# Performance work log

Measured on AMD Instinct MI355X. Metric: run time of the kernel, lower is better.

## Reference

```python
import jax, jax.numpy as jnp
import numpy as np

N, E, D, H, C, G = 20000, 160000, 128, 4, 3, 512
IN_F, EF = 74, 11


def setup_inputs():
    key = jax.random.key(0)
    ks = jax.random.split(key, 20)
    rn = lambda k, shape, s=0.05: jax.random.normal(k, shape, jnp.float32) * s
    return {
        "h0": rn(ks[0], (N, IN_F), 1.0),
        "e_f": rn(ks[1], (E, EF), 1.0),
        "src": jax.random.randint(ks[2], (E,), 0, N, jnp.int32),
        "dst": jax.random.randint(ks[3], (E,), 0, N, jnp.int32),
        "node_gid": jnp.sort(jax.random.randint(ks[4], (N,), 0, G, jnp.int32)),
        "num_graphs": G,
        "lin0_W": rn(ks[5], (H, IN_F, D)),
        "lin_W": rn(ks[6], (C - 1, H, D, D)),
        "We_W": rn(ks[7], (C, H, EF, D)),
        "Wq_W": rn(ks[8], (C, H, D, D)),
        "Wk_W": rn(ks[9], (C, H, D, D)),
        "Wv_W": rn(ks[10], (C, H, D, D)),
        "ln_g": jnp.ones((C, H, D), jnp.float32),
        "ln_b": jnp.zeros((C, H, D), jnp.float32),
        "out_W": rn(ks[11], (C, H * D, D)),
        "out_b": jnp.zeros((C, D), jnp.float32),
        "proj_W": rn(ks[12], (IN_F, D)),
        "proj_b": jnp.zeros((D,), jnp.float32),
        "gru_Wih0": rn(ks[13], (2, D, 3 * D)),
        "gru_Whh0": rn(ks[14], (2, D, 3 * D)),
        "gru_bih0": jnp.zeros((2, 3 * D), jnp.float32),
        "gru_bhh0": jnp.zeros((2, 3 * D), jnp.float32),
        "gru_Wih1": rn(ks[15], (2, 2 * D, 3 * D)),
        "gru_Whh1": rn(ks[16], (2, D, 3 * D)),
        "gru_bih1": jnp.zeros((2, 3 * D), jnp.float32),
        "gru_bhh1": jnp.zeros((2, 3 * D), jnp.float32),
    }


def _seg_mean(x, ids, n):
    s = jax.ops.segment_sum(x, ids, num_segments=n)
    c = jax.ops.segment_sum(jnp.ones((x.shape[0], 1), x.dtype), ids, num_segments=n)
    return s / jnp.maximum(c, 1.0)


def _layernorm(x, g, b, eps=1e-5):
    m = jnp.mean(x, -1, keepdims=True)
    v = jnp.var(x, -1, keepdims=True)
    return (x - m) * jax.lax.rsqrt(v + eps) * g + b


def _gat_head(h, ef_raw, src, dst, n, Wl, We, Wq, Wk, Wv, g, b):
    z = h @ Wl                                  # [N, D]
    ef = ef_raw @ We                            # [E, D]
    x = jnp.stack([z[src], z[dst], ef], axis=1)  # [E, 3, D]
    Q = jnp.einsum('eid,df->eif', x, Wq)
    K = jnp.einsum('eid,df->eif', x, Wk)
    V = jnp.einsum('eid,df->eif', x, Wv)
    attn = jax.nn.softmax(jnp.einsum('eid,ejd->eij', Q, K), axis=-1)  # [E,3,3]
    m = jnp.einsum('eij,ejd->ed', attn, V)      # (attn @ V).sum(1)
    h_new = _seg_mean(m, dst, n)                # mean over incoming edges
    return _layernorm(jax.nn.relu(h_new), g, b)


def _gru_dir(xs, Wih, Whh, bih, bhh, reverse):
    # xs: [T, B, in]; torch gate order r, z, n
    def step(h, x):
        gi = x @ Wih + bih
        gh = h @ Whh + bhh
        ir, iz, inn = jnp.split(gi, 3, axis=-1)
        hr, hz, hn = jnp.split(gh, 3, axis=-1)
        r = jax.nn.sigmoid(ir + hr)
        zg = jax.nn.sigmoid(iz + hz)
        ng = jnp.tanh(inn + r * hn)
        h_new = (1.0 - zg) * ng + zg * h
        return h_new, h_new
    h0 = jnp.zeros((xs.shape[1], Whh.shape[0]), xs.dtype)
    hT, ys = jax.lax.scan(step, h0, xs, reverse=reverse)
    return hT, ys


def _forward(h0, e_f, lin0_W, lin_W, We_W, Wq_W, Wk_W, Wv_W, ln_g, ln_b,
             out_W, out_b, proj_W, proj_b,
             gru_Wih0, gru_Whh0, gru_bih0, gru_bhh0,
             gru_Wih1, gru_Whh1, gru_bih1, gru_bhh1,
             src, dst, node_gid, num_graphs):
    n = h0.shape[0]
    conv_nums, head_nums = We_W.shape[0], We_W.shape[1]
    gru_list = [_seg_mean(h0, node_gid, num_graphs)]
    h = h0
    for j in range(conv_nums):
        heads = [_gat_head(h, e_f, src, dst, n,
                           lin0_W[i] if j == 0 else lin_W[j - 1, i],
                           We_W[j, i], Wq_W[j, i], Wk_W[j, i], Wv_W[j, i],
                           ln_g[j, i], ln_b[j, i])
                 for i in range(head_nums)]
        h = jnp.concatenate(heads, axis=1) @ out_W[j] + out_b[j]
        gru_list.append(_seg_mean(h, node_gid, num_graphs))
    # GRU readout: project initial 74-dim readout, seq = [proj, h1..hC]
    x0 = gru_list[0] @ proj_W + proj_b
    seq = jnp.stack([x0] + gru_list[1:], axis=0)  # [T, G, D]
    hf0, yf0 = _gru_dir(seq, gru_Wih0[0], gru_Whh0[0], gru_bih0[0], gru_bhh0[0], False)
    hb0, yb0 = _gru_dir(seq, gru_Wih0[1], gru_Whh0[1], gru_bih0[1], gru_bhh0[1], True)
    seq1 = jnp.concatenate([yf0, yb0], axis=-1)   # [T, G, 2D]
    hf1, _ = _gru_dir(seq1, gru_Wih1[0], gru_Whh1[0], gru_bih1[0], gru_bhh1[0], False)
    hb1, _ = _gru_dir(seq1, gru_Wih1[1], gru_Whh1[1], gru_bih1[1], gru_bhh1[1], True)
    # torch returns sum over the [num_layers*2, G, D] final hidden stack
    return hf0 + hb0 + hf1 + hb1


def reference(h0, e_f, src, dst, node_gid, num_graphs, lin0_W, lin_W, We_W,
              Wq_W, Wk_W, Wv_W, ln_g, ln_b, out_W, out_b, proj_W, proj_b,
              gru_Wih0, gru_Whh0, gru_bih0, gru_bhh0,
              gru_Wih1, gru_Whh1, gru_bih1, gru_bhh1):
    return _forward(h0, e_f, lin0_W, lin_W, We_W, Wq_W, Wk_W, Wv_W, ln_g, ln_b,
                    out_W, out_b, proj_W, proj_b,
                    gru_Wih0, gru_Whh0, gru_bih0, gru_bhh0,
                    gru_Wih1, gru_Whh1, gru_bih1, gru_bhh1,
                    src, dst, node_gid, num_graphs)
```

## Files before the change

kernel.cpp:

```cpp
#include <hip/hip_runtime.h>
#include <cstdint>

#define D_   128
#define H_   4
#define C_   3
#define G_   512
#define INF_ 74
#define EF_  11
#define T_   4
#define NW_  48

typedef __attribute__((ext_vector_type(8))) short bf16x8;
typedef __attribute__((ext_vector_type(4))) float f32x4;

__device__ inline unsigned short f2bf(float x) {
  unsigned u = __float_as_uint(x);
  unsigned r = u + 0x7fffu + ((u >> 16) & 1u);
  return (unsigned short)(r >> 16);
}
__device__ inline float bf2f(unsigned short x) {
  return __uint_as_float(((unsigned)x) << 16);
}
__device__ inline void unpack8(uint4 u, float* f) {
  f[0] = __uint_as_float(u.x << 16); f[1] = __uint_as_float(u.x & 0xffff0000u);
  f[2] = __uint_as_float(u.y << 16); f[3] = __uint_as_float(u.y & 0xffff0000u);
  f[4] = __uint_as_float(u.z << 16); f[5] = __uint_as_float(u.z & 0xffff0000u);
  f[6] = __uint_as_float(u.w << 16); f[7] = __uint_as_float(u.w & 0xffff0000u);
}

struct WDesc { const float* src; unsigned short* dst; int K; int D; int trans; };
struct WPack { WDesc d[NW_]; };

__global__ __launch_bounds__(256) void k_wcvt(WPack wp)
{
  WDesc w = wp.d[blockIdx.y];
  int tot = w.K * w.D;
  for (int i = blockIdx.x * 256 + threadIdx.x; i < tot; i += gridDim.x * 256) {
    if (w.trans) {
      int d = i / w.K, k = i - d * w.K;
      w.dst[i] = f2bf(w.src[(size_t)k * w.D + d]);
    } else {
      w.dst[i] = f2bf(w.src[i]);
    }
  }
}

__global__ __launch_bounds__(128) void k_small1(
    const float* __restrict__ WeW, const float* __restrict__ WqW,
    const float* __restrict__ WkW, const float* __restrict__ WvW,
    float* __restrict__ WeQ, float* __restrict__ WeK, float* __restrict__ WeV,
    float* __restrict__ GqT, float* __restrict__ GcT)
{
  int ch = blockIdx.x, f = blockIdx.y;
  const float* We = WeW + (size_t)ch * EF_ * 128 + f * 128;
  const float* Wq = WqW + (size_t)ch * 16384;
  const float* Wk = WkW + (size_t)ch * 16384;
  const float* Wv = WvW + (size_t)ch * 16384;
  __shared__ float sWe[128], sQ[128], sK[128];
  int d = threadIdx.x;
  sWe[d] = We[d];
  __syncthreads();
  float aq = 0.f, ak = 0.f, av = 0.f;
  for (int k = 0; k < 128; k++) {
    float w = sWe[k];
    aq += w * Wq[k * 128 + d];
    ak += w * Wk[k * 128 + d];
    av += w * Wv[k * 128 + d];
  }
  size_t off = (size_t)ch * EF_ * 128 + f * 128 + d;
  WeQ[off] = aq; WeK[off] = ak; WeV[off] = av;
  sQ[d] = aq; sK[d] = ak;
  __syncthreads();
  float gq = 0.f, gc = 0.f;
  for (int k = 0; k < 128; k++) {
    gq += Wq[(size_t)d * 128 + k] * sK[k];
    gc += Wk[(size_t)d * 128 + k] * sQ[k];
  }
  GqT[off] = gq; GcT[off] = gc;
}

__global__ __launch_bounds__(128) void k_small2(
    const float* __restrict__ WeQ, const float* __restrict__ WeK,
    float* __restrict__ M2)
{
  int ch = blockIdx.x;
  __shared__ float sQ[EF_ * 128], sK[EF_ * 128];
  int t = threadIdx.x;
  for (int i = t; i < EF_ * 128; i += 128) {
    sQ[i] = WeQ[(size_t)ch * EF_ * 128 + i];
    sK[i] = WeK[(size_t)ch * EF_ * 128 + i];
  }
  __syncthreads();
  if (t < EF_ * EF_) {
    int a = t / EF_, b = t % EF_;
    float s = 0.f;
    for (int k = 0; k < 128; k++) s += sQ[a * 128 + k] * sK[b * 128 + k];
    M2[(size_t)ch * (EF_ * EF_) + t] = s;
  }
}

__global__ __launch_bounds__(256) void k_utbt(
    const float* __restrict__ Mbuf, const float* __restrict__ GqT,
    const float* __restrict__ GcT, unsigned short* __restrict__ UTBt)
{
  int ch = blockIdx.x, slot = blockIdx.y;
  unsigned short* dst = UTBt + (size_t)ch * 49152 + slot * 16384;
  for (int i = threadIdx.x; i < 16384; i += 256) {
    int r = i >> 7, k = i & 127;
    float v;
    if (slot == 0)      v = Mbuf[(size_t)ch * 16384 + i];
    else if (slot == 1) v = Mbuf[(size_t)ch * 16384 + k * 128 + r];
    else v = (r < EF_) ? GqT[(size_t)ch * EF_ * 128 + r * 128 + k]
          : (r < 2 * EF_) ? GcT[(size_t)ch * EF_ * 128 + (r - EF_) * 128 + k] : 0.f;
    dst[i] = f2bf(v);
  }
}

template <typename AT>
__global__ __launch_bounds__(256) void k_mfma(
    const AT* __restrict__ A, int lda, int aOffZ, int M, int K,
    const unsigned short* __restrict__ Bt, int btOffY, int btOffZ,
    float* __restrict__ outF, int ldc, int cOffY, int cOffZ,
    const float* __restrict__ bias,
    unsigned short* __restrict__ outH, int hStride, int hOffY, int hOffZ)
{
  const int bx = blockIdx.x, by = blockIdx.y, bz = blockIdx.z;
  A += (size_t)bz * aOffZ;
  const unsigned short* Bp = Bt + (size_t)by * btOffY + (size_t)bz * btOffZ;
  const int rowBase = bx * 128;
  __shared__ unsigned short As[128][40];
  __shared__ unsigned short Bs[128][40];
  const int t = threadIdx.x;
  const int w = t >> 6, l = t & 63;
  const int wr = w >> 1, wc = w & 1;
  const int fr = l & 15, fq = l >> 4;
  f32x4 acc[4][4];
#pragma unroll
  for (int m = 0; m < 4; m++)
#pragma unroll
    for (int n = 0; n < 4; n++) acc[m][n] = (f32x4){0.f, 0.f, 0.f, 0.f};

  const int sr = t >> 1, sh = t & 1;
  const int arow = rowBase + sr;
  const AT* aBase = A + (size_t)arow * lda;

  for (int k0 = 0; k0 < K; k0 += 32) {
    int kb = k0 + sh * 16;
    if constexpr (sizeof(AT) == 4) {
      unsigned short tmp[16];
      if (arow < M && kb + 16 <= K) {
        const AT* ap = aBase + kb;
#pragma unroll
        for (int i = 0; i < 16; i++) tmp[i] = f2bf(ap[i]);
      } else {
#pragma unroll
        for (int i = 0; i < 16; i++) {
          int gk = kb + i;
          float v = (arow < M && gk < K) ? (float)aBase[gk] : 0.f;
          tmp[i] = f2bf(v);
        }
      }
      *(uint4*)&As[sr][sh * 16]     = *(const uint4*)&tmp[0];
      *(uint4*)&As[sr][sh * 16 + 8] = *(const uint4*)&tmp[8];
    } else {
      if (arow < M && kb + 16 <= K) {
        const unsigned short* ap = (const unsigned short*)aBase + kb;
        *(uint4*)&As[sr][sh * 16]     = *(const uint4*)(ap);
        *(uint4*)&As[sr][sh * 16 + 8] = *(const uint4*)(ap + 8);
      } else {
#pragma unroll
        for (int i = 0; i < 16; i++) {
          int gk = kb + i;
          As[sr][sh * 16 + i] = (arow < M && gk < K)
              ? ((const unsigned short*)aBase)[gk] : (unsigned short)0;
        }
      }
    }
    if (t < 128) {
      unsigned short tmp[32];
      if (k0 + 32 <= K) {
        const unsigned short* bp = Bp + (size_t)t * K + k0;
#pragma unroll
        for (int i = 0; i < 32; i++) tmp[i] = bp[i];
      } else {
#pragma unroll
        for (int i = 0; i < 32; i++) {
          int gk = k0 + i;
          tmp[i] = (gk < K) ? Bp[(size_t)t * K + gk] : (unsigned short)0;
        }
      }
#pragma unroll
      for (int i = 0; i < 4; i++) *(uint4*)&Bs[t][i * 8] = *(const uint4*)&tmp[i * 8];
    }
    __syncthreads();
    bf16x8 af[4], bfr[4];
#pragma unroll
    for (int m = 0; m < 4; m++) af[m]  = *(const bf16x8*)&As[wr * 64 + m * 16 + fr][fq * 8];
#pragma unroll
    for (int n = 0; n < 4; n++) bfr[n] = *(const bf16x8*)&Bs[wc * 64 + n * 16 + fr][fq * 8];
#pragma unroll
    for (int m = 0; m < 4; m++)
#pragma unroll
      for (int n = 0; n < 4; n++)
        acc[m][n] = __builtin_amdgcn_mfma_f32_16x16x32_bf16(af[m], bfr[n], acc[m][n], 0, 0, 0);
    __syncthreads();
  }
#pragma unroll
  for (int m = 0; m < 4; m++) {
    int row0 = rowBase + wr * 64 + m * 16 + fq * 4;
#pragma unroll
    for (int n = 0; n < 4; n++) {
      int col = wc * 64 + n * 16 + fr;
#pragma unroll
      for (int r = 0; r < 4; r++) {
        int row = row0 + r;
        if (row < M) {
          float v = acc[m][n][r];
          if (outH) {
            outH[(size_t)row * hStride + by * hOffY + bz * hOffZ + col] = f2bf(v);
          } else {
            if (bias) v += bias[col];
            outF[(size_t)row * ldc + by * cOffY + bz * cOffZ + col] = v;
          }
        }
      }
    }
  }
}

__global__ void k_hist(const int* __restrict__ dst, int* __restrict__ deg, int E)
{
  int e = blockIdx.x * blockDim.x + threadIdx.x;
  if (e < E) atomicAdd(&deg[dst[e]], 1);
}

__global__ __launch_bounds__(1024) void k_scan(const int* __restrict__ deg,
                                               int* __restrict__ rowp, int N)
{
  __shared__ int part[1024];
  int t = threadIdx.x;
  int chunk = (N + 1023) / 1024;
  int base = t * chunk;
  int s = 0;
  for (int i = 0; i < chunk; i++) { int idx = base + i; if (idx < N) s += deg[idx]; }
  part[t] = s;
  __syncthreads();
  for (int off = 1; off < 1024; off <<= 1) {
    int v = (t >= off) ? part[t - off] : 0;
    __syncthreads();
    part[t] += v;
    __syncthreads();
  }
  int run = part[t] - s;
  for (int i = 0; i < chunk; i++) {
    int idx = base + i;
    if (idx < N) { rowp[idx] = run; run += deg[idx]; }
  }
  if (t == 1023) rowp[N] = part[1023];
}

__global__ void k_fill(const int* __restrict__ src, const int* __restrict__ dst,
                       const int* __restrict__ rowp, int* __restrict__ cursor,
                       int* __restrict__ eids, int* __restrict__ src_perm,
                       int* __restrict__ dst_perm, int E)
{
  int e = blockIdx.x * blockDim.x + threadIdx.x;
  if (e < E) {
    int d = dst[e];
    int pos = atomicAdd(&cursor[d], 1);
    int slot = rowp[d] + pos;
    eids[slot] = e;
    src_perm[slot] = src[e];
    dst_perm[slot] = d;
  }
}

__global__ void k_efperm(const float* __restrict__ e_f, const int* __restrict__ eids,
                         float* __restrict__ ef_perm, int E)
{
  int i = blockIdx.x * blockDim.x + threadIdx.x;
  if (i < E * EF_) {
    int idx = i / EF_, f = i - idx * EF_;
    ef_perm[i] = e_f[(size_t)eids[idx] * EF_ + f];
  }
}

__global__ __launch_bounds__(128) void k_wve(
    const float* __restrict__ WvW, const float* __restrict__ WeV,
    unsigned short* __restrict__ WvE)
{
  int ch = blockIdx.x;
  const float* Wv  = WvW + (size_t)ch * 16384;
  const float* wev = WeV + (size_t)ch * EF_ * 128;
  unsigned short* dst = WvE + (size_t)ch * 20480;
  for (int i = threadIdx.x; i < 20480; i += 128) {
    int d = i / 160, k = i - d * 160;
    float v = (k < 128) ? Wv[(size_t)k * 128 + d]
            : (k < 128 + EF_) ? wev[(size_t)(k - 128) * 128 + d] : 0.f;
    dst[i] = f2bf(v);
  }
}

__global__ __launch_bounds__(256) void k_ss(
    const unsigned short* __restrict__ Zb, const unsigned short* __restrict__ UTb,
    float* __restrict__ ss, int N)
{
  int h = threadIdx.x >> 6, lane = threadIdx.x & 63;
  int n = blockIdx.x;
  unsigned uz = *(const unsigned*)(Zb + (size_t)n * 512 + h * 128 + 2 * lane);
  unsigned uu = *(const unsigned*)(UTb + (size_t)n * 1536 + h * 384 + 2 * lane);
  float zx = __uint_as_float(uz << 16), zy = __uint_as_float(uz & 0xffff0000u);
  float ux = __uint_as_float(uu << 16), uy = __uint_as_float(uu & 0xffff0000u);
  float p = zx * ux + zy * uy;
#pragma unroll
  for (int m = 32; m; m >>= 1) p += __shfl_xor(p, m, 64);
  if (lane == 0) ss[n * H_ + h] = p;
}

__global__ __launch_bounds__(256) void k_elog(
    const unsigned short* __restrict__ UTb, const float* __restrict__ ss,
    const float* __restrict__ M2, const float* __restrict__ ef_perm,
    const int* __restrict__ src_perm, const int* __restrict__ dst_perm,
    float* __restrict__ elog, int E, int layer)
{
  int i0 = blockIdx.x * 64;
  __shared__ float efs[64 * EF_];
  __shared__ float m2s[4 * EF_ * EF_];
  int t = threadIdx.x;
  for (int i = t; i < 64 * EF_; i += 256) {
    int gi = i0 * EF_ + i;
    efs[i] = (gi < E * EF_) ? ef_perm[gi] : 0.f;
  }
  for (int i = t; i < 4 * EF_ * EF_; i += 256)
    m2s[i] = M2[(size_t)layer * 4 * EF_ * EF_ + i];
  __syncthreads();
  int sl = t >> 2, h = t & 3;
  int idx = i0 + sl;
  if (idx < E) {
    int s = src_perm[idx], d = dst_perm[idx];
    const float* ef = &efs[sl * EF_];
    const float* m2 = &m2s[h * EF_ * EF_];
    float ee = 0.f;
#pragma unroll
    for (int a = 0; a < EF_; a++) {
      float r = 0.f;
#pragma unroll
      for (int b = 0; b < EF_; b++) r += m2[a * EF_ + b] * ef[b];
      ee += ef[a] * r;
    }
    const unsigned short* bs = UTb + (size_t)s * 1536 + h * 384 + 256;
    const unsigned short* cs = bs + EF_;
    const unsigned short* bd = UTb + (size_t)d * 1536 + h * 384 + 256;
    const unsigned short* cd = bd + EF_;
    float se = 0.f, es = 0.f, de = 0.f, ed = 0.f;
#pragma unroll
    for (int f = 0; f < EF_; f++) {
      float e = ef[f];
      se += bf2f(bs[f]) * e;
      es += bf2f(cs[f]) * e;
      de += bf2f(bd[f]) * e;
      ed += bf2f(cd[f]) * e;
    }
    float* o = elog + ((size_t)idx * H_ + h) * 6;
    o[0] = ss[s * H_ + h];
    o[1] = se; o[2] = de; o[3] = es; o[4] = ed; o[5] = ee;
  }
}

__global__ __launch_bounds__(256) void k_edge(
    const unsigned short* __restrict__ Zb, const unsigned short* __restrict__ UTb,
    const float* __restrict__ ss, const float* __restrict__ elog,
    const float* __restrict__ ef_perm, const int* __restrict__ rowp,
    const int* __restrict__ src_perm, unsigned short* __restrict__ aggZE, int N)
{
  const int h = threadIdx.x >> 6;
  const int lane = threadIdx.x & 63;
  const int q = lane & 15;
  const int g = lane >> 4;
  const int lb = lane & 48;
  const int n = blockIdx.x;

  float zd[8], ud[8], td[8];
  unpack8(*(const uint4*)(Zb + (size_t)n * 512 + h * 128 + q * 8), zd);
  const unsigned short* utp = UTb + (size_t)n * 1536 + h * 384 + q * 8;
  unpack8(*(const uint4*)(utp), ud);
  unpack8(*(const uint4*)(utp + 128), td);
  const float essd = __expf(ss[n * H_ + h]);
  const int beg = rowp[n], end = rowp[n + 1];
  float acc[8];
#pragma unroll
  for (int i = 0; i < 8; i++) acc[i] = 0.f;
  float wdsum = 0.f, a11 = 0.f;

  for (int idx0 = beg; idx0 < end; idx0 += 4) {
    int idxg = idx0 + g;
    bool act = idxg < end;
    int idxc = act ? idxg : beg;
    int s = src_perm[idxc];
    float zs[8];
    unpack8(*(const uint4*)(Zb + (size_t)s * 512 + h * 128 + q * 8), zs);
    float v1 = 0.f, v2 = 0.f;
#pragma unroll
    for (int i = 0; i < 8; i++) {
      v1 += zs[i] * ud[i];
      v2 += zs[i] * td[i];
    }
#pragma unroll
    for (int m = 1; m < 16; m <<= 1) {
      v1 += __shfl_xor(v1, m, 64);
      v2 += __shfl_xor(v2, m, 64);
    }
    float lv = (q < 6) ? elog[((size_t)idxc * H_ + h) * 6 + q] : 0.f;
    float S00 = __shfl(lv, lb + 0, 64);
    float S02 = __shfl(lv, lb + 1, 64);
    float S12 = __shfl(lv, lb + 2, 64);
    float S20 = __shfl(lv, lb + 3, 64);
    float S21 = __shfl(lv, lb + 4, 64);
    float S22 = __shfl(lv, lb + 5, 64);
    float e00 = __expf(S00), e01 = __expf(v1), e02 = __expf(S02);
    float i0r = 1.f / (e00 + e01 + e02);
    float e10 = __expf(v2), e12 = __expf(S12);
    float i1r = 1.f / (e10 + essd + e12);
    float e20 = __expf(S20), e21 = __expf(S21), e22 = __expf(S22);
    float i2r = 1.f / (e20 + e21 + e22);
    float w0 = e00 * i0r + e10 * i1r + e20 * i2r;
    float w1 = e01 * i0r + essd * i1r + e21 * i2r;
    float w2 = e02 * i0r + e12 * i1r + e22 * i2r;
    if (!act) { w0 = 0.f; w1 = 0.f; w2 = 0.f; }
#pragma unroll
    for (int i = 0; i < 8; i++) acc[i] += w0 * zs[i];
    wdsum += w1;
    float efl = (q < EF_) ? ef_perm[(size_t)idxc * EF_ + q] : 0.f;
    a11 += w2 * efl;
  }
#pragma unroll
  for (int m = 16; m < 64; m <<= 1) {
#pragma unroll
    for (int i = 0; i < 8; i++) acc[i] += __shfl_xor(acc[i], m, 64);
    wdsum += __shfl_xor(wdsum, m, 64);
    a11 += __shfl_xor(a11, m, 64);
  }
  int cnt = end - beg;
  float invc = (cnt > 0) ? 1.f / (float)cnt : 1.f;
  unsigned short* ob = aggZE + (size_t)n * 640 + h * 160;
  if (g == 0) {
    unsigned short tmp[8];
#pragma unroll
    for (int i = 0; i < 8; i++) tmp[i] = f2bf((acc[i] + wdsum * zd[i]) * invc);
    *(uint4*)(ob + q * 8) = *(const uint4*)&tmp[0];
    ob[128 + q] = (q < EF_) ? f2bf(a11 * invc) : (unsigned short)0;
  } else if (g == 1) {
    ob[144 + q] = 0;
  }
}

__global__ __launch_bounds__(256) void k_ln(
    float* __restrict__ zh, const float* __restrict__ lng,
    const float* __restrict__ lnb, int N, int layer)
{
  int h = threadIdx.x >> 6, lane = threadIdx.x & 63;
  int n = blockIdx.x;
  float* p = zh + (size_t)n * 512 + h * 128 + 2 * lane;
  float2 v = *(const float2*)p;
  v.x = fmaxf(v.x, 0.f); v.y = fmaxf(v.y, 0.f);
  float s1 = v.x + v.y;
#pragma unroll
  for (int m = 32; m; m >>= 1) s1 += __shfl_xor(s1, m, 64);
  float mean = s1 * (1.f / 128.f);
  float dx = v.x - mean, dy = v.y - mean;
  float s2 = dx * dx + dy * dy;
#pragma unroll
  for (int m = 32; m; m >>= 1) s2 += __shfl_xor(s2, m, 64);
  float rstd = rsqrtf(s2 * (1.f / 128.f) + 1e-5f);
  int gi = (layer * H_ + h) * 128 + 2 * lane;
  float2 g2 = *(const float2*)&lng[gi];
  float2 b2 = *(const float2*)&lnb[gi];
  float2 o;
  o.x = dx * rstd * g2.x + b2.x;
  o.y = dy * rstd * g2.y + b2.y;
  *(float2*)p = o;
}

__global__ void k_gmean(const float* __restrict__ X, const int* __restrict__ gid,
                        float* __restrict__ outp, int N, int ld)
{
  int g = blockIdx.x, part = blockIdx.y;
  int lo = 0, hi = N;
  while (lo < hi) { int m = (lo + hi) >> 1; if (gid[m] < g) lo = m + 1; else hi = m; }
  int s0 = lo;
  lo = s0; hi = N;
  while (lo < hi) { int m = (lo + hi) >> 1; if (gid[m] < g + 1) lo = m + 1; else hi = m; }
  int s1 = lo;
  int cnt = s1 - s0;
  float inv = 1.f / (float)(cnt > 0 ? cnt : 1);
  int r0 = s0 + (cnt * part) / 4;
  int r1 = s0 + (cnt * (part + 1)) / 4;
  if (r1 <= r0) return;
  for (int d = threadIdx.x; d < ld; d += blockDim.x) {
    float s = 0.f;
    for (int n = r0; n < r1; n++) s += X[(size_t)n * ld + d];
    atomicAdd(&outp[(size_t)g * ld + d], s * inv);
  }
}

__global__ __launch_bounds__(384) void k_gruR(
    const float* __restrict__ gi, const float* __restrict__ Whh,
    const float* __restrict__ bih, const float* __restrict__ bhh,
    float* __restrict__ yout, float* __restrict__ hfinal)
{
  const int g = blockIdx.x, dir = blockIdx.y, t = threadIdx.x;
  const float* W = Whh + (size_t)dir * 128 * 384 + t;
  const float bi = bih[dir * 384 + t];
  const float bh = bhh[dir * 384 + t];
  __shared__ float hb[128];
  __shared__ float rb[128], zb[128], nb[128];
  if (t < 128) hb[t] = 0.f;
  __syncthreads();
  for (int st = 0; st < T_; st++) {
    int ts = dir ? (T_ - 1 - st) : st;
    float acc = bh;
    for (int k = 0; k < 128; k++) acc += hb[k] * W[(size_t)k * 384];
    float gv = gi[((size_t)ts * G_ + g) * 768 + dir * 384 + t] + bi;
    if (t < 128) {
      rb[t] = 1.f / (1.f + __expf(-(gv + acc)));
    } else if (t < 256) {
      zb[t - 128] = 1.f / (1.f + __expf(-(gv + acc)));
    }
    __syncthreads();
    if (t >= 256) nb[t - 256] = tanhf(gv + rb[t - 256] * acc);
    __syncthreads();
    if (t < 128) {
      float z = zb[t];
      float h = (1.f - z) * nb[t] + z * hb[t];
      hb[t] = h;
      if (yout) yout[((size_t)ts * G_ + g) * 256 + dir * 128 + t] = h;
    }
    __syncthreads();
  }
  if (t < 128) hfinal[((size_t)dir * G_ + g) * 128 + t] = hb[t];
}

__global__ void k_final(const float* __restrict__ fp, float* __restrict__ outp, int n)
{
  int i = blockIdx.x * blockDim.x + threadIdx.x;
  if (i < n) {
    outp[i] = fp[i] + fp[G_ * 128 + i] + fp[2 * G_ * 128 + i] + fp[3 * G_ * 128 + i];
  }
}

extern "C" void kernel_launch(void* const* d_in, const int* in_sizes, int n_in,
                              void* d_out, int out_size, void* d_ws, size_t ws_size,
                              hipStream_t stream)
{
  (void)n_in; (void)ws_size;
  const float* h0   = (const float*)d_in[0];
  const float* e_f  = (const float*)d_in[1];
  const int*   srcI = (const int*)d_in[2];
  const int*   dstI = (const int*)d_in[3];
  const int*   gid  = (const int*)d_in[4];
  const float* lin0 = (const float*)d_in[6];
  const float* linW = (const float*)d_in[7];
  const float* WeW  = (const float*)d_in[8];
  const float* WqW  = (const float*)d_in[9];
  const float* WkW  = (const float*)d_in[10];
  const float* WvW  = (const float*)d_in[11];
  const float* lng  = (const float*)d_in[12];
  const float* lnb  = (const float*)d_in[13];
  const float* outW = (const float*)d_in[14];
  const float* outb = (const float*)d_in[15];
  const float* projW= (const float*)d_in[16];
  const float* projb= (const float*)d_in[17];
  const float* Wih0 = (const float*)d_in[18];
  const float* Whh0 = (const float*)d_in[19];
  const float* bih0 = (const float*)d_in[20];
  const float* bhh0 = (const float*)d_in[21];
  const float* Wih1 = (const float*)d_in[22];
  const float* Whh1 = (const float*)d_in[23];
  const float* bih1 = (const float*)d_in[24];
  const float* bhh1 = (const float*)d_in[25];
  float* outp = (float*)d_out;

  const int N = in_sizes[0] / INF_;
  const int E = in_sizes[2];

  char* wp = (char*)d_ws;
  auto alloc = [&](size_t bytes) -> void* {
    void* p = (void*)wp;
    wp += (bytes + 255) & ~(size_t)255;
    return p;
  };
  unsigned short* Zb  = (unsigned short*)alloc((size_t)N * 512 * 2);
  unsigned short* UTb = (unsigned short*)alloc((size_t)N * 1536 * 2);
  unsigned short* aggZE = (unsigned short*)alloc((size_t)N * 640 * 2);
  float* zh   = (float*)alloc((size_t)N * 512 * 4);
  float* hcur = (float*)alloc((size_t)N * 128 * 4);
  float* ssb  = (float*)alloc((size_t)N * H_ * 4);
  float* elog = (float*)alloc((size_t)E * H_ * 6 * 4);
  float* efp  = (float*)alloc((size_t)E * EF_ * 4);
  float* WeQ  = (float*)alloc((size_t)C_ * H_ * EF_ * 128 * 4);
  float* WeK  = (float*)alloc((size_t)C_ * H_ * EF_ * 128 * 4);
  float* WeV  = (float*)alloc((size_t)C_ * H_ * EF_ * 128 * 4);
  float* M2   = (float*)alloc((size_t)C_ * H_ * EF_ * EF_ * 4);
  float* GqT  = (float*)alloc((size_t)C_ * H_ * EF_ * 128 * 4);
  float* GcT  = (float*)alloc((size_t)C_ * H_ * EF_ * 128 * 4);
  float* Mbuf = (float*)alloc((size_t)C_ * H_ * 16384 * 4);
  unsigned short* WkPl  = (unsigned short*)alloc((size_t)C_ * H_ * 16384 * 2);
  unsigned short* UTBt  = (unsigned short*)alloc((size_t)C_ * H_ * 3 * 16384 * 2);
  unsigned short* WvE   = (unsigned short*)alloc((size_t)C_ * H_ * 20480 * 2);
  unsigned short* linBt0 = (unsigned short*)alloc((size_t)4 * 128 * INF_ * 2);
  unsigned short* linBt12= (unsigned short*)alloc((size_t)2 * 512 * 128 * 2);
  unsigned short* outBt  = (unsigned short*)alloc((size_t)C_ * 128 * 512 * 2);
  unsigned short* projBt = (unsigned short*)alloc((size_t)128 * INF_ * 2);
  unsigned short* WihBt0 = (unsigned short*)alloc((size_t)768 * 128 * 2);
  unsigned short* WihBt1 = (unsigned short*)alloc((size_t)768 * 256 * 2);
  float* gibuf = (float*)alloc((size_t)T_ * G_ * 768 * 4);
  int* deg    = (int*)alloc((size_t)N * 4);
  int* cursor = (int*)alloc((size_t)N * 4);
  int* rowp   = (int*)alloc((size_t)(N + 1) * 4);
  int* eids   = (int*)alloc((size_t)E * 4);
  int* srcp   = (int*)alloc((size_t)E * 4);
  int* dstp   = (int*)alloc((size_t)E * 4);
  float* gm74 = (float*)alloc((size_t)G_ * INF_ * 4);
  float* seq  = (float*)alloc((size_t)T_ * G_ * 128 * 4);
  float* seq1 = (float*)alloc((size_t)T_ * G_ * 256 * 4);
  float* fparts=(float*)alloc((size_t)4 * G_ * 128 * 4);

  const int gM = (N + 127) / 128;

  hipMemsetAsync(deg, 0, (size_t)N * 4, stream);
  hipMemsetAsync(cursor, 0, (size_t)N * 4, stream);
  hipMemsetAsync(gm74, 0, (size_t)G_ * INF_ * 4, stream);
  hipMemsetAsync(seq, 0, (size_t)T_ * G_ * 128 * 4, stream);
  k_hist<<<(E + 255) / 256, 256, 0, stream>>>(dstI, deg, E);
  k_scan<<<1, 1024, 0, stream>>>(deg, rowp, N);
  k_fill<<<(E + 255) / 256, 256, 0, stream>>>(srcI, dstI, rowp, cursor,
                                              eids, srcp, dstp, E);
  k_efperm<<<(E * EF_ + 255) / 256, 256, 0, stream>>>(e_f, eids, efp, E);

  k_small1<<<dim3(C_ * H_, EF_), 128, 0, stream>>>(WeW, WqW, WkW, WvW,
                                                   WeQ, WeK, WeV, GqT, GcT);
  k_small2<<<C_ * H_, 128, 0, stream>>>(WeQ, WeK, M2);
  k_wve<<<C_ * H_, 128, 0, stream>>>(WvW, WeV, WvE);

  {
    WPack w{};
    int nw = 0;
    auto addw = [&](const float* s, unsigned short* d, int K, int D, int tr) {
      w.d[nw].src = s; w.d[nw].dst = d; w.d[nw].K = K; w.d[nw].D = D;
      w.d[nw].trans = tr; nw++;
    };
    for (int h = 0; h < 4; h++)
      addw(lin0 + (size_t)h * INF_ * 128, linBt0 + (size_t)h * 128 * INF_, INF_, 128, 1);
    for (int j = 1; j < 3; j++)
      for (int h = 0; h < 4; h++)
        addw(linW + ((size_t)(j - 1) * 4 + h) * 16384,
             linBt12 + (size_t)(j - 1) * 65536 + (size_t)h * 16384, 128, 128, 1);
    for (int j = 0; j < 3; j++)
      addw(outW + (size_t)j * 65536, outBt + (size_t)j * 65536, 512, 128, 1);
    addw(projW, projBt, INF_, 128, 1);
    for (int ch = 0; ch < 12; ch++)
      addw(WkW + (size_t)ch * 16384, WkPl + (size_t)ch * 16384, 128, 128, 0);
    for (int dir = 0; dir < 2; dir++) {
      addw(Wih0 + (size_t)dir * 128 * 384, WihBt0 + (size_t)dir * 384 * 128,
           128, 384, 1);
      addw(Wih1 + (size_t)dir * 256 * 384, WihBt1 + (size_t)dir * 384 * 256,
           256, 384, 1);
    }
    k_wcvt<<<dim3(64, nw), 256, 0, stream>>>(w);
  }

  k_mfma<float><<<dim3(1, 1, 12), 256, 0, stream>>>(
      WqW, 128, 16384, 128, 128, WkPl, 0, 16384,
      Mbuf, 128, 0, 16384, nullptr, nullptr, 0, 0, 0);

  k_utbt<<<dim3(12, 3), 256, 0, stream>>>(Mbuf, GqT, GcT, UTBt);

  k_gmean<<<dim3(G_, 4), 128, 0, stream>>>(h0, gid, gm74, N, INF_);
  k_mfma<float><<<dim3(4, 1, 1), 256, 0, stream>>>(
      gm74, INF_, 0, G_, INF_, projBt, 0, 0,
      seq, 128, 0, 0, projb, nullptr, 0, 0, 0);

  for (int j = 0; j < C_; j++) {
    if (j == 0)
      k_mfma<float><<<dim3(gM, 4, 1), 256, 0, stream>>>(
          h0, INF_, 0, N, INF_, linBt0, 128 * INF_, 0,
          nullptr, 0, 0, 0, nullptr, Zb, 512, 128, 0);
    else
      k_mfma<float><<<dim3(gM, 4, 1), 256, 0, stream>>>(
          hcur, 128, 0, N, 128, linBt12 + (size_t)(j - 1) * 65536, 16384, 0,
          nullptr, 0, 0, 0, nullptr, Zb, 512, 128, 0);
    k_mfma<unsigned short><<<dim3(gM, 3, 4), 256, 0, stream>>>(
        Zb, 512, 128, N, 128, UTBt + (size_t)j * 4 * 49152, 16384, 49152,
        nullptr, 0, 0, 0, nullptr, UTb, 1536, 128, 384);
    k_ss<<<N, 256, 0, stream>>>(Zb, UTb, ssb, N);
    k_elog<<<(E + 63) / 64, 256, 0, stream>>>(UTb, ssb, M2, efp, srcp, dstp,
                                              elog, E, j);
    k_edge<<<N, 256, 0, stream>>>(Zb, UTb, ssb, elog, efp, rowp, srcp, aggZE, N);
    k_mfma<unsigned short><<<dim3(gM, 1, 4), 256, 0, stream>>>(
        aggZE, 640, 160, N, 160, WvE + (size_t)j * 4 * 20480, 0, 20480,
        zh, 512, 0, 128, nullptr, nullptr, 0, 0, 0);
    k_ln<<<N, 256, 0, stream>>>(zh, lng, lnb, N, j);
    k_mfma<float><<<dim3(gM, 1, 1), 256, 0, stream>>>(
        zh, 512, 0, N, 512, outBt + (size_t)j * 65536, 0, 0,
        hcur, 128, 0, 0, outb + j * 128, nullptr, 0, 0, 0);
    k_gmean<<<dim3(G_, 4), 128, 0, stream>>>(hcur, gid,
                                             seq + (size_t)(j + 1) * G_ * 128, N, 128);
  }

  k_mfma<float><<<dim3(16, 6, 1), 256, 0, stream>>>(
      seq, 128, 0, T_ * G_, 128, WihBt0, 128 * 128, 0,
      gibuf, 768, 128, 0, nullptr, nullptr, 0, 0, 0);
  k_gruR<<<dim3(G_, 2), 384, 0, stream>>>(gibuf, Whh0, bih0, bhh0,
                                          seq1, fparts);
  k_mfma<float><<<dim3(16, 6, 1), 256, 0, stream>>>(
      seq1, 256, 0, T_ * G_, 256, WihBt1, 128 * 256, 0,
      gibuf, 768, 128, 0, nullptr, nullptr, 0, 0, 0);
  k_gruR<<<dim3(G_, 2), 384, 0, stream>>>(gibuf, Whh1, bih1, bhh1,
                                          nullptr, fparts + 2 * G_ * 128);
  k_final<<<(out_size + 255) / 256, 256, 0, stream>>>(fparts, outp, out_size);
}
```

Measured before the change: 1.237 ms.

## Fold edge-feature projections into lin weights and split edge loop across waves

Precomputes lin_W·Gq/Gc products into a compact per-layer weight (k_bcfold), so the 22 edge-feature coefficient columns per head come from one small GEMM on the layer input instead of a third 128-wide slot in the Z·UT GEMM. This shrinks UTb from 1536 to 1024 columns per node and gives k_elog a compact 128-wide BCb buffer to gather from. k_edge is also restructured: each wave now handles all four heads for one edge, with waves striding over edges and a shared-memory reduction at the end, replacing per-head waves that processed four edges each. The cost is an extra small GEMM per layer, bf16 rounding of the folded weights, and a block-wide sync in k_edge.

```diff
diff --git a/kernel.cpp b/kernel.cpp
--- a/kernel.cpp
+++ b/kernel.cpp
@@ -100,19 +100,44 @@
 }
 
 __global__ __launch_bounds__(256) void k_utbt(
-    const float* __restrict__ Mbuf, const float* __restrict__ GqT,
-    const float* __restrict__ GcT, unsigned short* __restrict__ UTBt)
+    const float* __restrict__ Mbuf, unsigned short* __restrict__ UTBt)
 {
   int ch = blockIdx.x, slot = blockIdx.y;
-  unsigned short* dst = UTBt + (size_t)ch * 49152 + slot * 16384;
+  unsigned short* dst = UTBt + (size_t)ch * 32768 + slot * 16384;
   for (int i = threadIdx.x; i < 16384; i += 256) {
     int r = i >> 7, k = i & 127;
-    float v;
-    if (slot == 0)      v = Mbuf[(size_t)ch * 16384 + i];
-    else if (slot == 1) v = Mbuf[(size_t)ch * 16384 + k * 128 + r];
-    else v = (r < EF_) ? GqT[(size_t)ch * EF_ * 128 + r * 128 + k]
-          : (r < 2 * EF_) ? GcT[(size_t)ch * EF_ * 128 + (r - EF_) * 128 + k] : 0.f;
+    float v = (slot == 0) ? Mbuf[(size_t)ch * 16384 + i]
+                          : Mbuf[(size_t)ch * 16384 + k * 128 + r];
     dst[i] = f2bf(v);
+  }
+}
+
+__global__ __launch_bounds__(128) void k_bcfold(
+    const float* __restrict__ lin0, const float* __restrict__ linW,
+    const float* __restrict__ GqT, const float* __restrict__ GcT,
+    unsigned short* __restrict__ Wbc)
+{
+  int j = blockIdx.x, col = blockIdx.y;
+  int K = (j == 0) ? INF_ : 128;
+  int h = col >> 5, c2 = col & 31;
+  __shared__ float sG[128];
+  int t = threadIdx.x;
+  if (c2 < 2 * EF_) {
+    int f = (c2 < EF_) ? c2 : c2 - EF_;
+    const float* G = ((c2 < EF_) ? GqT : GcT) +
+                     ((size_t)(j * H_ + h) * EF_ + f) * 128;
+    sG[t] = G[t];
+  }
+  __syncthreads();
+  if (t < K) {
+    float v = 0.f;
+    if (c2 < 2 * EF_) {
+      const float* lin = (j == 0)
+          ? lin0 + (size_t)h * INF_ * 128 + t * 128
+          : linW + ((size_t)(j - 1) * H_ + h) * 16384 + t * 128;
+      for (int d = 0; d < 128; d++) v += lin[d] * sG[d];
+    }
+    Wbc[(size_t)j * 16384 + col * K + t] = f2bf(v);
   }
 }
 
@@ -308,7 +333,7 @@
   int h = threadIdx.x >> 6, lane = threadIdx.x & 63;
   int n = blockIdx.x;
   unsigned uz = *(const unsigned*)(Zb + (size_t)n * 512 + h * 128 + 2 * lane);
-  unsigned uu = *(const unsigned*)(UTb + (size_t)n * 1536 + h * 384 + 2 * lane);
+  unsigned uu = *(const unsigned*)(UTb + (size_t)n * 1024 + h * 256 + 2 * lane);
   float zx = __uint_as_float(uz << 16), zy = __uint_as_float(uz & 0xffff0000u);
   float ux = __uint_as_float(uu << 16), uy = __uint_as_float(uu & 0xffff0000u);
   float p = zx * ux + zy * uy;
@@ -318,7 +343,7 @@
 }
 
 __global__ __launch_bounds__(256) void k_elog(
-    const unsigned short* __restrict__ UTb, const float* __restrict__ ss,
+    const unsigned short* __restrict__ BCb, const float* __restrict__ ss,
     const float* __restrict__ M2, const float* __restrict__ ef_perm,
     const int* __restrict__ src_perm, const int* __restrict__ dst_perm,
     float* __restrict__ elog, int E, int layer)
@@ -348,18 +373,16 @@
       for (int b = 0; b < EF_; b++) r += m2[a * EF_ + b] * ef[b];
       ee += ef[a] * r;
     }
-    const unsigned short* bs = UTb + (size_t)s * 1536 + h * 384 + 256;
-    const unsigned short* cs = bs + EF_;
-    const unsigned short* bd = UTb + (size_t)d * 1536 + h * 384 + 256;
-    const unsigned short* cd = bd + EF_;
+    const unsigned short* bs = BCb + (size_t)s * 128 + h * 32;
+    const unsigned short* bd = BCb + (size_t)d * 128 + h * 32;
     float se = 0.f, es = 0.f, de = 0.f, ed = 0.f;
 #pragma unroll
     for (int f = 0; f < EF_; f++) {
       float e = ef[f];
       se += bf2f(bs[f]) * e;
-      es += bf2f(cs[f]) * e;
+      es += bf2f(bs[EF_ + f]) * e;
       de += bf2f(bd[f]) * e;
-      ed += bf2f(cd[f]) * e;
+      ed += bf2f(bd[EF_ + f]) * e;
     }
     float* o = elog + ((size_t)idx * H_ + h) * 6;
     o[0] = ss[s * H_ + h];
@@ -373,16 +396,16 @@
     const float* __restrict__ ef_perm, const int* __restrict__ rowp,
     const int* __restrict__ src_perm, unsigned short* __restrict__ aggZE, int N)
 {
-  const int h = threadIdx.x >> 6;
+  const int w = threadIdx.x >> 6;
   const int lane = threadIdx.x & 63;
+  const int h = lane >> 4;
   const int q = lane & 15;
-  const int g = lane >> 4;
   const int lb = lane & 48;
   const int n = blockIdx.x;
 
   float zd[8], ud[8], td[8];
-  unpack8(*(const uint4*)(Zb + (size_t)n * 512 + h * 128 + q * 8), zd);
-  const unsigned short* utp = UTb + (size_t)n * 1536 + h * 384 + q * 8;
+  unpack8(*(const uint4*)(Zb + (size_t)n * 512 + lane * 8), zd);
+  const unsigned short* utp = UTb + (size_t)n * 1024 + h * 256 + q * 8;
   unpack8(*(const uint4*)(utp), ud);
   unpack8(*(const uint4*)(utp + 128), td);
   const float essd = __expf(ss[n * H_ + h]);
@@ -392,13 +415,10 @@
   for (int i = 0; i < 8; i++) acc[i] = 0.f;
   float wdsum = 0.f, a11 = 0.f;
 
-  for (int idx0 = beg; idx0 < end; idx0 += 4) {
-    int idxg = idx0 + g;
-    bool act = idxg < end;
-    int idxc = act ? idxg : beg;
-    int s = src_perm[idxc];
+  for (int idx = beg + w; idx < end; idx += 4) {
+    int s = src_perm[idx];
     float zs[8];
-    unpack8(*(const uint4*)(Zb + (size_t)s * 512 + h * 128 + q * 8), zs);
+    unpack8(*(const uint4*)(Zb + (size_t)s * 512 + lane * 8), zs);
     float v1 = 0.f, v2 = 0.f;
 #pragma unroll
     for (int i = 0; i < 8; i++) {
@@ -410,7 +430,7 @@
       v1 += __shfl_xor(v1, m, 64);
       v2 += __shfl_xor(v2, m, 64);
     }
-    float lv = (q < 6) ? elog[((size_t)idxc * H_ + h) * 6 + q] : 0.f;
+    float lv = (q < 6) ? elog[((size_t)idx * H_ + h) * 6 + q] : 0.f;
     float S00 = __shfl(lv, lb + 0, 64);
     float S02 = __shfl(lv, lb + 1, 64);
     float S12 = __shfl(lv, lb + 2, 64);
@@ -426,30 +446,33 @@
     float w0 = e00 * i0r + e10 * i1r + e20 * i2r;
     float w1 = e01 * i0r + essd * i1r + e21 * i2r;
     float w2 = e02 * i0r + e12 * i1r + e22 * i2r;
-    if (!act) { w0 = 0.f; w1 = 0.f; w2 = 0.f; }
 #pragma unroll
     for (int i = 0; i < 8; i++) acc[i] += w0 * zs[i];
     wdsum += w1;
-    float efl = (q < EF_) ? ef_perm[(size_t)idxc * EF_ + q] : 0.f;
+    float efl = (q < EF_) ? ef_perm[(size_t)idx * EF_ + q] : 0.f;
     a11 += w2 * efl;
   }
-#pragma unroll
-  for (int m = 16; m < 64; m <<= 1) {
-#pragma unroll
-    for (int i = 0; i < 8; i++) acc[i] += __shfl_xor(acc[i], m, 64);
-    wdsum += __shfl_xor(wdsum, m, 64);
-    a11 += __shfl_xor(a11, m, 64);
-  }
-  int cnt = end - beg;
-  float invc = (cnt > 0) ? 1.f / (float)cnt : 1.f;
-  unsigned short* ob = aggZE + (size_t)n * 640 + h * 160;
-  if (g == 0) {
+  __shared__ float red[4][64][10];
+#pragma unroll
+  for (int i = 0; i < 8; i++) red[w][lane][i] = acc[i];
+  red[w][lane][8] = wdsum;
+  red[w][lane][9] = a11;
+  __syncthreads();
+  if (w == 0) {
+    float a[8], wd = 0.f, a1 = 0.f;
+#pragma unroll
+    for (int i = 0; i < 8; i++)
+      a[i] = red[0][lane][i] + red[1][lane][i] + red[2][lane][i] + red[3][lane][i];
+    wd = red[0][lane][8] + red[1][lane][8] + red[2][lane][8] + red[3][lane][8];
+    a1 = red[0][lane][9] + red[1][lane][9] + red[2][lane][9] + red[3][lane][9];
+    int cnt = end - beg;
+    float invc = (cnt > 0) ? 1.f / (float)cnt : 1.f;
+    unsigned short* ob = aggZE + (size_t)n * 640 + h * 160;
     unsigned short tmp[8];
 #pragma unroll
-    for (int i = 0; i < 8; i++) tmp[i] = f2bf((acc[i] + wdsum * zd[i]) * invc);
+    for (int i = 0; i < 8; i++) tmp[i] = f2bf((a[i] + wd * zd[i]) * invc);
     *(uint4*)(ob + q * 8) = *(const uint4*)&tmp[0];
-    ob[128 + q] = (q < EF_) ? f2bf(a11 * invc) : (unsigned short)0;
-  } else if (g == 1) {
+    ob[128 + q] = (q < EF_) ? f2bf(a1 * invc) : (unsigned short)0;
     ob[144 + q] = 0;
   }
 }
@@ -590,7 +613,8 @@
     return p;
   };
   unsigned short* Zb  = (unsigned short*)alloc((size_t)N * 512 * 2);
-  unsigned short* UTb = (unsigned short*)alloc((size_t)N * 1536 * 2);
+  unsigned short* UTb = (unsigned short*)alloc((size_t)N * 1024 * 2);
+  unsigned short* BCb = (unsigned short*)alloc((size_t)N * 128 * 2);
   unsigned short* aggZE = (unsigned short*)alloc((size_t)N * 640 * 2);
   float* zh   = (float*)alloc((size_t)N * 512 * 4);
   float* hcur = (float*)alloc((size_t)N * 128 * 4);
@@ -605,7 +629,8 @@
   float* GcT  = (float*)alloc((size_t)C_ * H_ * EF_ * 128 * 4);
   float* Mbuf = (float*)alloc((size_t)C_ * H_ * 16384 * 4);
   unsigned short* WkPl  = (unsigned short*)alloc((size_t)C_ * H_ * 16384 * 2);
-  unsigned short* UTBt  = (unsigned short*)alloc((size_t)C_ * H_ * 3 * 16384 * 2);
+  unsigned short* UTBt  = (unsigned short*)alloc((size_t)C_ * H_ * 2 * 16384 * 2);
+  unsigned short* WbcBt = (unsigned short*)alloc((size_t)C_ * 16384 * 2);
   unsigned short* WvE   = (unsigned short*)alloc((size_t)C_ * H_ * 20480 * 2);
   unsigned short* linBt0 = (unsigned short*)alloc((size_t)4 * 128 * INF_ * 2);
   unsigned short* linBt12= (unsigned short*)alloc((size_t)2 * 512 * 128 * 2);
@@ -641,6 +666,7 @@
                                                    WeQ, WeK, WeV, GqT, GcT);
   k_small2<<<C_ * H_, 128, 0, stream>>>(WeQ, WeK, M2);
   k_wve<<<C_ * H_, 128, 0, stream>>>(WvW, WeV, WvE);
+  k_bcfold<<<dim3(C_, 128), 128, 0, stream>>>(lin0, linW, GqT, GcT, WbcBt);
 
   {
     WPack w{};
@@ -673,7 +699,7 @@
       WqW, 128, 16384, 128, 128, WkPl, 0, 16384,
       Mbuf, 128, 0, 16384, nullptr, nullptr, 0, 0, 0);
 
-  k_utbt<<<dim3(12, 3), 256, 0, stream>>>(Mbuf, GqT, GcT, UTBt);
+  k_utbt<<<dim3(12, 2), 256, 0, stream>>>(Mbuf, UTBt);
 
   k_gmean<<<dim3(G_, 4), 128, 0, stream>>>(h0, gid, gm74, N, INF_);
   k_mfma<float><<<dim3(4, 1, 1), 256, 0, stream>>>(
@@ -681,6 +707,8 @@
       seq, 128, 0, 0, projb, nullptr, 0, 0, 0);
 
   for (int j = 0; j < C_; j++) {
+    const float* Ain = (j == 0) ? h0 : hcur;
+    const int Kin = (j == 0) ? INF_ : 128;
     if (j == 0)
       k_mfma<float><<<dim3(gM, 4, 1), 256, 0, stream>>>(
           h0, INF_, 0, N, INF_, linBt0, 128 * INF_, 0,
@@ -689,11 +717,14 @@
       k_mfma<float><<<dim3(gM, 4, 1), 256, 0, stream>>>(
           hcur, 128, 0, N, 128, linBt12 + (size_t)(j - 1) * 65536, 16384, 0,
           nullptr, 0, 0, 0, nullptr, Zb, 512, 128, 0);
-    k_mfma<unsigned short><<<dim3(gM, 3, 4), 256, 0, stream>>>(
-        Zb, 512, 128, N, 128, UTBt + (size_t)j * 4 * 49152, 16384, 49152,
-        nullptr, 0, 0, 0, nullptr, UTb, 1536, 128, 384);
+    k_mfma<float><<<dim3(gM, 1, 1), 256, 0, stream>>>(
+        Ain, Kin, 0, N, Kin, WbcBt + (size_t)j * 16384, 0, 0,
+        nullptr, 0, 0, 0, nullptr, BCb, 128, 0, 0);
+    k_mfma<unsigned short><<<dim3(gM, 2, 4), 256, 0, stream>>>(
+        Zb, 512, 128, N, 128, UTBt + (size_t)j * 4 * 32768, 16384, 32768,
+        nullptr, 0, 0, 0, nullptr, UTb, 1024, 128, 256);
     k_ss<<<N, 256, 0, stream>>>(Zb, UTb, ssb, N);
-    k_elog<<<(E + 63) / 64, 256, 0, stream>>>(UTb, ssb, M2, efp, srcp, dstp,
+    k_elog<<<(E + 63) / 64, 256, 0, stream>>>(BCb, ssb, M2, efp, srcp, dstp,
                                               elog, E, j);
     k_edge<<<N, 256, 0, stream>>>(Zb, UTb, ssb, elog, efp, rowp, srcp, aggZE, N);
     k_mfma<unsigned short><<<dim3(gM, 1, 4), 256, 0, stream>>>(
```

Measured after the change: 1.168 ms. -5.5%, faster.
